# Optimization experiments

Measured on AMD Instinct MI355X. Metric: run time of the kernel, lower is better.

The kernel has to match this reference:

```python
import jax, jax.numpy as jnp
import numpy as np

B, C, H, W = 8, 512, 32, 32
HEADS, GROUPS = 8, 32
EPS = 1e-5


def setup_inputs() -> dict:
    key = jax.random.key(0)
    ks = jax.random.split(key, 6)
    s = 0.02
    return {
        "x": jax.random.normal(ks[0], (B, C, H, W), jnp.float32),
        "gn_scale": jnp.ones((C,), jnp.float32),
        "gn_bias": jnp.zeros((C,), jnp.float32),
        "wq": jax.random.normal(ks[1], (C, C), jnp.float32) * s,
        "bq": jnp.zeros((C,), jnp.float32),
        "wk": jax.random.normal(ks[2], (C, C), jnp.float32) * s,
        "bk": jnp.zeros((C,), jnp.float32),
        "wv": jax.random.normal(ks[3], (C, C), jnp.float32) * s,
        "bv": jnp.zeros((C,), jnp.float32),
        "wo": jax.random.normal(ks[4], (C, C), jnp.float32) * s,
        "bo": jnp.zeros((C,), jnp.float32),
    }


def reference(x, gn_scale, gn_bias, wq, bq, wk, bk, wv, bv, wo, bo):
    b, c, h, w = x.shape
    n = h * w
    cdh = c // HEADS
    xf = x.reshape(b, c, n)

    # GroupNorm over (channels_per_group, spatial)
    g = xf.reshape(b, GROUPS, (c // GROUPS) * n)
    mu = g.mean(-1, keepdims=True)
    var = g.var(-1, keepdims=True)
    hn = ((g - mu) * jax.lax.rsqrt(var + EPS)).reshape(b, c, n)
    hn = hn * gn_scale[:, None] + gn_bias[:, None]

    # 1x1 conv projections == channel-mixing GEMMs
    q = jnp.einsum('oc,bcn->bon', wq, hn) + bq[:, None]
    k = jnp.einsum('oc,bcn->bon', wk, hn) + bk[:, None]
    v = jnp.einsum('oc,bcn->bon', wv, hn) + bv[:, None]

    qh = q.reshape(b, HEADS, cdh, n)
    kh = k.reshape(b, HEADS, cdh, n)
    vh = v.reshape(b, HEADS, cdh, n)

    scale = 1.0 / jnp.sqrt(jnp.float32(cdh))
    scores = jnp.einsum('bhdq,bhdk->bhqk', qh, kh) * scale  # [B,H,N,N]
    attn = jax.nn.softmax(scores, axis=-1)  # dropout p=0.0 (eval) -> identity

    oh = jnp.einsum('bhqk,bhdk->bhdq', attn, vh).reshape(b, c, n)
    out = jnp.einsum('oc,bcn->bon', wo, oh) + bo[:, None]
    return (xf + out).reshape(b, c, h, w)
```

## Files before the change

kernel.cpp:

```cpp
#include <hip/hip_runtime.h>

#define BB 8
#define CC 512
#define NSP 1024
#define HEADS 8
#define DH 64
#define NGROUPS 32
#define CPG 16
#define GN_EPS 1e-5f
#define MQKV 1536

typedef __attribute__((ext_vector_type(8))) short bf16x8;
typedef __attribute__((ext_vector_type(4))) short short4v;
typedef __attribute__((ext_vector_type(4))) float f32x4;

typedef __attribute__((address_space(3))) unsigned int lds_u32;
typedef const __attribute__((address_space(1))) unsigned int glb_u32;

__device__ __forceinline__ short f2bf(float f) {
    union { float f; unsigned u; } v; v.f = f;
    unsigned r = v.u + 0x7fffu + ((v.u >> 16) & 1u);
    return (short)(r >> 16);
}
__device__ __forceinline__ short f2bf_trunc(float f) {
    union { float f; unsigned u; } v; v.f = f;
    return (short)(v.u >> 16);
}

__device__ __forceinline__ float wave_reduce_sum(float v) {
    #pragma unroll
    for (int off = 32; off > 0; off >>= 1) v += __shfl_down(v, off, 64);
    return v;
}

#define QSCALE 0.18033688011112042f

__global__ __launch_bounds__(256) void convert_w_kernel(
        const float* __restrict__ wq, const float* __restrict__ wk,
        const float* __restrict__ wv, const float* __restrict__ wo,
        const float* __restrict__ bq, const float* __restrict__ bk,
        const float* __restrict__ bv,
        short* __restrict__ wqkv, short* __restrict__ wob,
        float* __restrict__ bqkv) {
    const int gid = blockIdx.x * 256 + threadIdx.x;
    if (gid < MQKV * CC) {
        const int r = gid >> 9;
        const int cc = gid & 511;
        const float* src = (r < 512) ? wq : ((r < 1024) ? wk : wv);
        float v = src[(size_t)(r & 511) * CC + cc];
        if (r < 512) v *= QSCALE;
        wqkv[gid] = f2bf(v);
    } else {
        const int g2 = gid - MQKV * CC;
        wob[g2] = f2bf(wo[g2]);
    }
    if (gid < MQKV) {
        float bvv = (gid < 512) ? bq[gid] * QSCALE
                  : ((gid < 1024) ? bk[gid - 512] : bv[gid - 1024]);
        bqkv[gid] = bvv;
    }
}

__global__ __launch_bounds__(256) void groupnorm_t_kernel(
        const float* __restrict__ x, const float* __restrict__ gsc,
        const float* __restrict__ gbi, short* __restrict__ hnt) {
    const int b = blockIdx.x >> 5, g = blockIdx.x & 31;
    const int count = CPG * NSP;
    const size_t base = ((size_t)b * CC + (size_t)g * CPG) * NSP;
    float s = 0.f, ss = 0.f;
    for (int i = threadIdx.x; i < count; i += 256) {
        float v = x[base + i];
        s += v; ss += v * v;
    }
    __shared__ float red[2][4];
    s = wave_reduce_sum(s); ss = wave_reduce_sum(ss);
    const int wid = threadIdx.x >> 6, lane = threadIdx.x & 63;
    if (lane == 0) { red[0][wid] = s; red[1][wid] = ss; }
    __syncthreads();
    if (threadIdx.x == 0) {
        float ts  = red[0][0] + red[0][1] + red[0][2] + red[0][3];
        float tss = red[1][0] + red[1][1] + red[1][2] + red[1][3];
        float mu = ts / count;
        float var = tss / count - mu * mu;
        red[0][0] = mu;
        red[1][0] = rsqrtf(var + GN_EPS);
    }
    __syncthreads();
    const float mu = red[0][0], rstd = red[1][0];
    float sc[16], bi[16];
    #pragma unroll
    for (int ci = 0; ci < 16; ++ci) {
        sc[ci] = gsc[g * CPG + ci] * rstd;
        bi[ci] = gbi[g * CPG + ci];
    }
    for (int n0 = 0; n0 < NSP; n0 += 256) {
        const int n = n0 + threadIdx.x;
        short tmp[16];
        #pragma unroll
        for (int ci = 0; ci < 16; ++ci) {
            float v = x[base + (size_t)ci * NSP + n];
            tmp[ci] = f2bf((v - mu) * sc[ci] + bi[ci]);
        }
        const size_t ob = ((size_t)b * NSP + n) * CC + g * CPG;
        *(bf16x8*)&hnt[ob]     = *(bf16x8*)&tmp[0];
        *(bf16x8*)&hnt[ob + 8] = *(bf16x8*)&tmp[8];
    }
}

template <int MODE>
__global__ __launch_bounds__(256) void gemm_bt_kernel(
        const short* __restrict__ A, const float* __restrict__ bias,
        const short* __restrict__ Bt, void* __restrict__ Yv,
        const float* __restrict__ res, short* __restrict__ qt,
        short* __restrict__ kt, int M) {
    __shared__ short SM[2 * 128 * 64];
    short* As = SM;
    short* Bs = SM + 128 * 64;
    const int nt = blockIdx.x;
    const int b = nt >> 3, n0 = (nt & 7) * 128;
    const int o0 = blockIdx.y * 128;
    const int t = threadIdx.x, w = t >> 6, lane = t & 63;
    const int quad = lane >> 4, l16 = lane & 15;
    const int wm = w & 1, wn = w >> 1;
    const int srow = lane >> 3, scol = (lane & 7) * 8;

    f32x4 acc[4][4];
    #pragma unroll
    for (int i = 0; i < 4; ++i)
        #pragma unroll
        for (int j = 0; j < 4; ++j) acc[i][j] = (f32x4){0.f, 0.f, 0.f, 0.f};

    const short* Ab = A + (size_t)o0 * 512;
    const short* Bb = Bt + ((size_t)b * 1024 + n0) * 512;

    for (int k0 = 0; k0 < 512; k0 += 64) {
        #pragma unroll
        for (int i = 0; i < 4; ++i) {
            const int r0 = w * 32 + i * 8;
            __builtin_amdgcn_global_load_lds(
                (glb_u32*)(Ab + (size_t)(r0 + srow) * 512 + k0 + scol),
                (lds_u32*)&As[r0 * 64], 16, 0, 0);
            __builtin_amdgcn_global_load_lds(
                (glb_u32*)(Bb + (size_t)(r0 + srow) * 512 + k0 + scol),
                (lds_u32*)&Bs[r0 * 64], 16, 0, 0);
        }
        __syncthreads();

        bf16x8 af[4][2], bfr[4][2];
        #pragma unroll
        for (int mi = 0; mi < 4; ++mi)
            #pragma unroll
            for (int s = 0; s < 2; ++s)
                af[mi][s] = *(bf16x8*)&As[(wm * 64 + mi * 16 + l16) * 64 + quad * 8 + s * 32];
        #pragma unroll
        for (int ni = 0; ni < 4; ++ni)
            #pragma unroll
            for (int s = 0; s < 2; ++s)
                bfr[ni][s] = *(bf16x8*)&Bs[(wn * 64 + ni * 16 + l16) * 64 + quad * 8 + s * 32];
        #pragma unroll
        for (int mi = 0; mi < 4; ++mi)
            #pragma unroll
            for (int ni = 0; ni < 4; ++ni)
                #pragma unroll
                for (int s = 0; s < 2; ++s)
                    acc[mi][ni] = __builtin_amdgcn_mfma_f32_16x16x32_bf16(
                        af[mi][s], bfr[ni][s], acc[mi][ni], 0, 0, 0);
        __syncthreads();
    }

    if (MODE == 0 && o0 < 1024) {
        short* T = (o0 < 512) ? qt : kt;
        #pragma unroll
        for (int pass = 0; pass < 2; ++pass) {
            __syncthreads();
            if (wm == pass) {
                #pragma unroll
                for (int mi = 0; mi < 4; ++mi) {
                    const int d0 = mi * 16 + quad * 4;
                    float bv[4];
                    #pragma unroll
                    for (int r = 0; r < 4; ++r) bv[r] = bias[o0 + pass * 64 + d0 + r];
                    #pragma unroll
                    for (int ni = 0; ni < 4; ++ni) {
                        const int nl = wn * 64 + ni * 16 + l16;
                        short pk[4];
                        #pragma unroll
                        for (int r = 0; r < 4; ++r)
                            pk[r] = f2bf(acc[mi][ni][r] + bv[r]);
                        *(short4v*)&SM[nl * 68 + d0] = *(short4v*)pk;
                    }
                }
            }
            __syncthreads();
            const int hh = ((o0 & 511) >> 6) + pass;
            const size_t hb2 = ((size_t)b * HEADS + hh) * NSP;
            #pragma unroll
            for (int it = 0; it < 4; ++it) {
                const int rr = (t >> 3) + it * 32;
                const int cc = (t & 7) * 8;
                *(bf16x8*)&T[(hb2 + n0 + rr) * DH + cc] = *(bf16x8*)&SM[rr * 68 + cc];
            }
        }
        return;
    }

    #pragma unroll
    for (int mi = 0; mi < 4; ++mi) {
        #pragma unroll
        for (int r = 0; r < 4; ++r) {
            const int m = wm * 64 + mi * 16 + quad * 4 + r;
            const float bv = bias[o0 + m];
            const size_t rowb = ((size_t)b * M + o0 + m) * 1024 + n0;
            if (MODE == 0) {
                short* Y = (short*)Yv;
                #pragma unroll
                for (int ni = 0; ni < 4; ++ni) {
                    const int n = wn * 64 + ni * 16 + l16;
                    Y[rowb + n] = f2bf(acc[mi][ni][r] + bv);
                }
            } else {
                float* Y = (float*)Yv;
                #pragma unroll
                for (int ni = 0; ni < 4; ++ni) {
                    const int n = wn * 64 + ni * 16 + l16;
                    Y[rowb + n] = acc[mi][ni][r] + bv + res[rowb + n];
                }
            }
        }
    }
}

__global__ __launch_bounds__(256) void attn_mfma_kernel(
        const short* __restrict__ qkv, const short* __restrict__ qt,
        const short* __restrict__ kt, short* __restrict__ obt) {
    __shared__ short Ks[64 * 64];
    __shared__ short Vs[64 * 64];
    __shared__ short Ps[4][32][68];
    const int id = blockIdx.x;
    const int xcd = id & 7, j = id >> 3;
    const int q0 = (j & 7) * 128;
    const int hi = (j >> 3) * 8 + xcd;
    const int b = hi >> 3, h = hi & 7;
    const int t = threadIdx.x;
    const int w = t >> 6, lane = t & 63;
    const int quad = lane >> 4, l16 = lane & 15;
    const size_t vbase = ((size_t)b * MQKV + 1024 + h * DH) * NSP;
    const size_t hb = ((size_t)b * HEADS + h) * NSP;
    const int sc = (lane & 7) ^ (lane >> 3);
    const int swz0 = (quad ^ (l16 & 7)) * 8;
    const int swz1 = ((quad + 4) ^ (l16 & 7)) * 8;

    bf16x8 qf[2][2];
    #pragma unroll
    for (int g = 0; g < 2; ++g)
        #pragma unroll
        for (int s = 0; s < 2; ++s)
            qf[g][s] = *(const bf16x8*)&qt[(hb + q0 + w * 32 + g * 16 + l16) * DH
                                           + quad * 8 + 32 * s];

    float lsum[2] = {0.f, 0.f};
    f32x4 oacc[2][4];
    #pragma unroll
    for (int g = 0; g < 2; ++g)
        #pragma unroll
        for (int i = 0; i < 4; ++i) oacc[g][i] = (f32x4){0.f, 0.f, 0.f, 0.f};

    for (int k0 = 0; k0 < NSP; k0 += 64) {
        __syncthreads();
        #pragma unroll
        for (int p = 0; p < 2; ++p) {
            const int row = w * 16 + p * 8 + (lane >> 3);
            __builtin_amdgcn_global_load_lds(
                (glb_u32*)(kt + (hb + k0 + row) * DH + sc * 8),
                (lds_u32*)(Ks + w * 1024 + p * 512), 16, 0, 0);
            __builtin_amdgcn_global_load_lds(
                (glb_u32*)(qkv + vbase + (size_t)row * NSP + k0 + sc * 8),
                (lds_u32*)(Vs + w * 1024 + p * 512), 16, 0, 0);
        }
        __syncthreads();

        f32x4 st[2][4];
        #pragma unroll
        for (int ks = 0; ks < 4; ++ks) {
            bf16x8 ka0 = *(bf16x8*)&Ks[(ks * 16 + l16) * 64 + swz0];
            bf16x8 ka1 = *(bf16x8*)&Ks[(ks * 16 + l16) * 64 + swz1];
            #pragma unroll
            for (int g = 0; g < 2; ++g) {
                f32x4 a2 = (f32x4){0.f, 0.f, 0.f, 0.f};
                a2 = __builtin_amdgcn_mfma_f32_16x16x32_bf16(ka0, qf[g][0], a2, 0, 0, 0);
                a2 = __builtin_amdgcn_mfma_f32_16x16x32_bf16(ka1, qf[g][1], a2, 0, 0, 0);
                st[g][ks] = a2;
            }
        }

        #pragma unroll
        for (int g = 0; g < 2; ++g) {
            short pb[16];
            #pragma unroll
            for (int ks = 0; ks < 4; ++ks)
                #pragma unroll
                for (int r = 0; r < 4; ++r) {
                    float p = exp2f(st[g][ks][r]);
                    lsum[g] += p;
                    pb[ks * 4 + r] = f2bf_trunc(p);
                }
            #pragma unroll
            for (int ks = 0; ks < 4; ++ks)
                *(short4v*)&Ps[w][g * 16 + l16][ks * 16 + quad * 4] = *(short4v*)&pb[ks * 4];
        }
        bf16x8 pf[2][2];
        #pragma unroll
        for (int g = 0; g < 2; ++g)
            #pragma unroll
            for (int s = 0; s < 2; ++s)
                pf[g][s] = *(bf16x8*)&Ps[w][g * 16 + l16][quad * 8 + 32 * s];

        #pragma unroll
        for (int ds = 0; ds < 4; ++ds) {
            bf16x8 va0 = *(bf16x8*)&Vs[(ds * 16 + l16) * 64 + swz0];
            bf16x8 va1 = *(bf16x8*)&Vs[(ds * 16 + l16) * 64 + swz1];
            #pragma unroll
            for (int g = 0; g < 2; ++g) {
                oacc[g][ds] = __builtin_amdgcn_mfma_f32_16x16x32_bf16(va0, pf[g][0], oacc[g][ds], 0, 0, 0);
                oacc[g][ds] = __builtin_amdgcn_mfma_f32_16x16x32_bf16(va1, pf[g][1], oacc[g][ds], 0, 0, 0);
            }
        }
    }

    #pragma unroll
    for (int g = 0; g < 2; ++g) {
        float ls = lsum[g];
        ls += __shfl_xor(ls, 16, 64);
        ls += __shfl_xor(ls, 32, 64);
        const float inv = 1.0f / ls;
        const int qrow = q0 + w * 32 + g * 16 + l16;
        #pragma unroll
        for (int ds = 0; ds < 4; ++ds) {
            short o4[4];
            #pragma unroll
            for (int r = 0; r < 4; ++r) o4[r] = f2bf(oacc[g][ds][r] * inv);
            *(short4v*)&obt[((size_t)b * NSP + qrow) * CC + h * DH + ds * 16 + quad * 4] =
                *(short4v*)o4;
        }
    }
}

extern "C" void kernel_launch(void* const* d_in, const int* in_sizes, int n_in,
                              void* d_out, int out_size, void* d_ws, size_t ws_size,
                              hipStream_t stream) {
    const float* x   = (const float*)d_in[0];
    const float* gsc = (const float*)d_in[1];
    const float* gbi = (const float*)d_in[2];
    const float* wq  = (const float*)d_in[3];
    const float* bq  = (const float*)d_in[4];
    const float* wk  = (const float*)d_in[5];
    const float* bk  = (const float*)d_in[6];
    const float* wv  = (const float*)d_in[7];
    const float* bv  = (const float*)d_in[8];
    const float* wo  = (const float*)d_in[9];
    const float* bo  = (const float*)d_in[10];
    float* out = (float*)d_out;

    short* wqkv_bf = (short*)d_ws;
    short* wo_bf   = wqkv_bf + (size_t)MQKV * CC;
    float* bqkv    = (float*)(wo_bf + (size_t)CC * CC);
    short* hnt     = (short*)(bqkv + MQKV);
    short* qkv     = hnt + (size_t)BB * NSP * CC;
    short* obt     = qkv + (size_t)BB * MQKV * NSP;
    short* kt      = obt + (size_t)BB * NSP * CC;
    short* qt      = kt + (size_t)BB * HEADS * NSP * DH;

    convert_w_kernel<<<(MQKV * CC + CC * CC) / 256, 256, 0, stream>>>(
        wq, wk, wv, wo, bq, bk, bv, wqkv_bf, wo_bf, bqkv);

    groupnorm_t_kernel<<<BB * NGROUPS, 256, 0, stream>>>(x, gsc, gbi, hnt);

    dim3 qkvgrid(64, MQKV / 128);
    gemm_bt_kernel<0><<<qkvgrid, 256, 0, stream>>>(
        wqkv_bf, bqkv, hnt, (void*)qkv, nullptr, qt, kt, MQKV);

    attn_mfma_kernel<<<512, 256, 0, stream>>>(qkv, qt, kt, obt);

    dim3 wogrid(64, CC / 128);
    gemm_bt_kernel<1><<<wogrid, 256, 0, stream>>>(
        wo_bf, bo, obt, (void*)out, x, nullptr, nullptr, CC);
}
```

Measured before the change: 193.2 us.

## Fuse groupnorm with weight conversion and shrink GEMM M-tile to 64

Merges weight conversion and groupnorm into one launch. Weight conversion now uses float4 loads, and groupnorm caches each group's input slab in LDS (64KB) so x is read from global memory once instead of twice. The GEMM tile drops from 128x128 to 64x128, which doubles the grid for better CU occupancy on the small projections. The Q/K transpose epilogue now goes through a per-wave swizzled LDS staging buffer with no block-wide barriers. The tradeoffs are 64KB of LDS per groupnorm block, which limits occupancy, and less operand reuse in the GEMM.

```diff
diff --git a/kernel.cpp b/kernel.cpp
--- a/kernel.cpp
+++ b/kernel.cpp
@@ -35,49 +35,59 @@
 
 #define QSCALE 0.18033688011112042f
 
-__global__ __launch_bounds__(256) void convert_w_kernel(
+__global__ __launch_bounds__(256) void gn_conv_kernel(
+        const float* __restrict__ x, const float* __restrict__ gsc,
+        const float* __restrict__ gbi, short* __restrict__ hnt,
         const float* __restrict__ wq, const float* __restrict__ wk,
         const float* __restrict__ wv, const float* __restrict__ wo,
         const float* __restrict__ bq, const float* __restrict__ bk,
         const float* __restrict__ bv,
         short* __restrict__ wqkv, short* __restrict__ wob,
         float* __restrict__ bqkv) {
-    const int gid = blockIdx.x * 256 + threadIdx.x;
-    if (gid < MQKV * CC) {
-        const int r = gid >> 9;
-        const int cc = gid & 511;
-        const float* src = (r < 512) ? wq : ((r < 1024) ? wk : wv);
-        float v = src[(size_t)(r & 511) * CC + cc];
-        if (r < 512) v *= QSCALE;
-        wqkv[gid] = f2bf(v);
-    } else {
-        const int g2 = gid - MQKV * CC;
-        wob[g2] = f2bf(wo[g2]);
-    }
-    if (gid < MQKV) {
-        float bvv = (gid < 512) ? bq[gid] * QSCALE
-                  : ((gid < 1024) ? bk[gid - 512] : bv[gid - 1024]);
-        bqkv[gid] = bvv;
-    }
-}
-
-__global__ __launch_bounds__(256) void groupnorm_t_kernel(
-        const float* __restrict__ x, const float* __restrict__ gsc,
-        const float* __restrict__ gbi, short* __restrict__ hnt) {
+    __shared__ float xs[CPG * NSP];
+    __shared__ float red[2][4];
+    const int t = threadIdx.x;
+
+    if (blockIdx.x >= 256) {
+        const int base = (blockIdx.x - 256) * 1024 + t * 4;
+        short pk[4];
+        if (base < MQKV * CC) {
+            const int r = base >> 9, cc = base & 511;
+            const float* src = (r < 512) ? wq : ((r < 1024) ? wk : wv);
+            float4 v = *(const float4*)&src[(size_t)(r & 511) * CC + cc];
+            if (r < 512) { v.x *= QSCALE; v.y *= QSCALE; v.z *= QSCALE; v.w *= QSCALE; }
+            pk[0] = f2bf(v.x); pk[1] = f2bf(v.y); pk[2] = f2bf(v.z); pk[3] = f2bf(v.w);
+            *(short4v*)&wqkv[base] = *(short4v*)pk;
+        } else {
+            const int g2 = base - MQKV * CC;
+            float4 v = *(const float4*)&wo[g2];
+            pk[0] = f2bf(v.x); pk[1] = f2bf(v.y); pk[2] = f2bf(v.z); pk[3] = f2bf(v.w);
+            *(short4v*)&wob[g2] = *(short4v*)pk;
+        }
+        const int fid = (blockIdx.x - 256) * 256 + t;
+        if (fid < MQKV) {
+            float bvv = (fid < 512) ? bq[fid] * QSCALE
+                      : ((fid < 1024) ? bk[fid - 512] : bv[fid - 1024]);
+            bqkv[fid] = bvv;
+        }
+        return;
+    }
+
     const int b = blockIdx.x >> 5, g = blockIdx.x & 31;
     const int count = CPG * NSP;
     const size_t base = ((size_t)b * CC + (size_t)g * CPG) * NSP;
     float s = 0.f, ss = 0.f;
-    for (int i = threadIdx.x; i < count; i += 256) {
-        float v = x[base + i];
-        s += v; ss += v * v;
-    }
-    __shared__ float red[2][4];
+    for (int i = t * 4; i < count; i += 1024) {
+        float4 v = *(const float4*)&x[base + i];
+        *(float4*)&xs[i] = v;
+        s += v.x + v.y + v.z + v.w;
+        ss += v.x * v.x + v.y * v.y + v.z * v.z + v.w * v.w;
+    }
     s = wave_reduce_sum(s); ss = wave_reduce_sum(ss);
-    const int wid = threadIdx.x >> 6, lane = threadIdx.x & 63;
+    const int wid = t >> 6, lane = t & 63;
     if (lane == 0) { red[0][wid] = s; red[1][wid] = ss; }
     __syncthreads();
-    if (threadIdx.x == 0) {
+    if (t == 0) {
         float ts  = red[0][0] + red[0][1] + red[0][2] + red[0][3];
         float tss = red[1][0] + red[1][1] + red[1][2] + red[1][3];
         float mu = ts / count;
@@ -94,11 +104,11 @@
         bi[ci] = gbi[g * CPG + ci];
     }
     for (int n0 = 0; n0 < NSP; n0 += 256) {
-        const int n = n0 + threadIdx.x;
+        const int n = n0 + t;
         short tmp[16];
         #pragma unroll
         for (int ci = 0; ci < 16; ++ci) {
-            float v = x[base + (size_t)ci * NSP + n];
+            float v = xs[ci * NSP + n];
             tmp[ci] = f2bf((v - mu) * sc[ci] + bi[ci]);
         }
         const size_t ob = ((size_t)b * NSP + n) * CC + g * CPG;
@@ -113,54 +123,56 @@
         const short* __restrict__ Bt, void* __restrict__ Yv,
         const float* __restrict__ res, short* __restrict__ qt,
         short* __restrict__ kt, int M) {
-    __shared__ short SM[2 * 128 * 64];
-    short* As = SM;
-    short* Bs = SM + 128 * 64;
+    __shared__ short As[64 * 64];
+    __shared__ short Bs[128 * 64];
     const int nt = blockIdx.x;
     const int b = nt >> 3, n0 = (nt & 7) * 128;
-    const int o0 = blockIdx.y * 128;
+    const int o0 = blockIdx.y * 64;
     const int t = threadIdx.x, w = t >> 6, lane = t & 63;
     const int quad = lane >> 4, l16 = lane & 15;
-    const int wm = w & 1, wn = w >> 1;
-    const int srow = lane >> 3, scol = (lane & 7) * 8;
-
-    f32x4 acc[4][4];
+
+    f32x4 acc[4][2];
     #pragma unroll
     for (int i = 0; i < 4; ++i)
         #pragma unroll
-        for (int j = 0; j < 4; ++j) acc[i][j] = (f32x4){0.f, 0.f, 0.f, 0.f};
+        for (int j = 0; j < 2; ++j) acc[i][j] = (f32x4){0.f, 0.f, 0.f, 0.f};
 
     const short* Ab = A + (size_t)o0 * 512;
     const short* Bb = Bt + ((size_t)b * 1024 + n0) * 512;
+    const int lrow = lane >> 3, lch = lane & 7;
 
     for (int k0 = 0; k0 < 512; k0 += 64) {
         #pragma unroll
-        for (int i = 0; i < 4; ++i) {
-            const int r0 = w * 32 + i * 8;
+        for (int p = 0; p < 2; ++p) {
+            const int row = w * 16 + p * 8 + lrow;
             __builtin_amdgcn_global_load_lds(
-                (glb_u32*)(Ab + (size_t)(r0 + srow) * 512 + k0 + scol),
-                (lds_u32*)&As[r0 * 64], 16, 0, 0);
+                (glb_u32*)(Ab + (size_t)row * 512 + k0 + lch * 8),
+                (lds_u32*)&As[(w * 2 + p) * 512], 16, 0, 0);
+        }
+        #pragma unroll
+        for (int p = 0; p < 4; ++p) {
+            const int row = w * 32 + p * 8 + lrow;
             __builtin_amdgcn_global_load_lds(
-                (glb_u32*)(Bb + (size_t)(r0 + srow) * 512 + k0 + scol),
-                (lds_u32*)&Bs[r0 * 64], 16, 0, 0);
+                (glb_u32*)(Bb + (size_t)row * 512 + k0 + lch * 8),
+                (lds_u32*)&Bs[(w * 4 + p) * 512], 16, 0, 0);
         }
         __syncthreads();
 
-        bf16x8 af[4][2], bfr[4][2];
+        bf16x8 af[4][2], bfr[2][2];
         #pragma unroll
         for (int mi = 0; mi < 4; ++mi)
             #pragma unroll
             for (int s = 0; s < 2; ++s)
-                af[mi][s] = *(bf16x8*)&As[(wm * 64 + mi * 16 + l16) * 64 + quad * 8 + s * 32];
-        #pragma unroll
-        for (int ni = 0; ni < 4; ++ni)
+                af[mi][s] = *(bf16x8*)&As[(mi * 16 + l16) * 64 + quad * 8 + s * 32];
+        #pragma unroll
+        for (int ni = 0; ni < 2; ++ni)
             #pragma unroll
             for (int s = 0; s < 2; ++s)
-                bfr[ni][s] = *(bf16x8*)&Bs[(wn * 64 + ni * 16 + l16) * 64 + quad * 8 + s * 32];
+                bfr[ni][s] = *(bf16x8*)&Bs[(w * 32 + ni * 16 + l16) * 64 + quad * 8 + s * 32];
         #pragma unroll
         for (int mi = 0; mi < 4; ++mi)
             #pragma unroll
-            for (int ni = 0; ni < 4; ++ni)
+            for (int ni = 0; ni < 2; ++ni)
                 #pragma unroll
                 for (int s = 0; s < 2; ++s)
                     acc[mi][ni] = __builtin_amdgcn_mfma_f32_16x16x32_bf16(
@@ -170,36 +182,30 @@
 
     if (MODE == 0 && o0 < 1024) {
         short* T = (o0 < 512) ? qt : kt;
-        #pragma unroll
-        for (int pass = 0; pass < 2; ++pass) {
-            __syncthreads();
-            if (wm == pass) {
-                #pragma unroll
-                for (int mi = 0; mi < 4; ++mi) {
-                    const int d0 = mi * 16 + quad * 4;
-                    float bv[4];
-                    #pragma unroll
-                    for (int r = 0; r < 4; ++r) bv[r] = bias[o0 + pass * 64 + d0 + r];
-                    #pragma unroll
-                    for (int ni = 0; ni < 4; ++ni) {
-                        const int nl = wn * 64 + ni * 16 + l16;
-                        short pk[4];
-                        #pragma unroll
-                        for (int r = 0; r < 4; ++r)
-                            pk[r] = f2bf(acc[mi][ni][r] + bv[r]);
-                        *(short4v*)&SM[nl * 68 + d0] = *(short4v*)pk;
-                    }
-                }
+        const int hh = (o0 & 511) >> 6;
+        const size_t hb2 = ((size_t)b * HEADS + hh) * NSP;
+        short* Ts = Bs + w * 2048;
+        #pragma unroll
+        for (int mi = 0; mi < 4; ++mi) {
+            const int d0 = mi * 16 + quad * 4;
+            const int c = d0 >> 3, dlo = d0 & 7;
+            float bv[4];
+            #pragma unroll
+            for (int r = 0; r < 4; ++r) bv[r] = bias[o0 + d0 + r];
+            #pragma unroll
+            for (int ni = 0; ni < 2; ++ni) {
+                const int nl = ni * 16 + l16;
+                short pk[4];
+                #pragma unroll
+                for (int r = 0; r < 4; ++r) pk[r] = f2bf(acc[mi][ni][r] + bv[r]);
+                *(short4v*)&Ts[nl * 64 + ((c ^ (nl & 7)) * 8) + dlo] = *(short4v*)pk;
             }
-            __syncthreads();
-            const int hh = ((o0 & 511) >> 6) + pass;
-            const size_t hb2 = ((size_t)b * HEADS + hh) * NSP;
-            #pragma unroll
-            for (int it = 0; it < 4; ++it) {
-                const int rr = (t >> 3) + it * 32;
-                const int cc = (t & 7) * 8;
-                *(bf16x8*)&T[(hb2 + n0 + rr) * DH + cc] = *(bf16x8*)&SM[rr * 68 + cc];
-            }
+        }
+        #pragma unroll
+        for (int it = 0; it < 4; ++it) {
+            const int rr = lrow + it * 8;
+            bf16x8 vv = *(bf16x8*)&Ts[rr * 64 + ((lch ^ (rr & 7)) * 8)];
+            *(bf16x8*)&T[(hb2 + n0 + w * 32 + rr) * DH + lch * 8] = vv;
         }
         return;
     }
@@ -208,21 +214,21 @@
     for (int mi = 0; mi < 4; ++mi) {
         #pragma unroll
         for (int r = 0; r < 4; ++r) {
-            const int m = wm * 64 + mi * 16 + quad * 4 + r;
+            const int m = mi * 16 + quad * 4 + r;
             const float bv = bias[o0 + m];
             const size_t rowb = ((size_t)b * M + o0 + m) * 1024 + n0;
             if (MODE == 0) {
                 short* Y = (short*)Yv;
                 #pragma unroll
-                for (int ni = 0; ni < 4; ++ni) {
-                    const int n = wn * 64 + ni * 16 + l16;
+                for (int ni = 0; ni < 2; ++ni) {
+                    const int n = w * 32 + ni * 16 + l16;
                     Y[rowb + n] = f2bf(acc[mi][ni][r] + bv);
                 }
             } else {
                 float* Y = (float*)Yv;
                 #pragma unroll
-                for (int ni = 0; ni < 4; ++ni) {
-                    const int n = wn * 64 + ni * 16 + l16;
+                for (int ni = 0; ni < 2; ++ni) {
+                    const int n = w * 32 + ni * 16 + l16;
                     Y[rowb + n] = acc[mi][ni][r] + bv + res[rowb + n];
                 }
             }
@@ -370,18 +376,16 @@
     short* kt      = obt + (size_t)BB * NSP * CC;
     short* qt      = kt + (size_t)BB * HEADS * NSP * DH;
 
-    convert_w_kernel<<<(MQKV * CC + CC * CC) / 256, 256, 0, stream>>>(
-        wq, wk, wv, wo, bq, bk, bv, wqkv_bf, wo_bf, bqkv);
-
-    groupnorm_t_kernel<<<BB * NGROUPS, 256, 0, stream>>>(x, gsc, gbi, hnt);
-
-    dim3 qkvgrid(64, MQKV / 128);
+    gn_conv_kernel<<<1280, 256, 0, stream>>>(
+        x, gsc, gbi, hnt, wq, wk, wv, wo, bq, bk, bv, wqkv_bf, wo_bf, bqkv);
+
+    dim3 qkvgrid(64, MQKV / 64);
     gemm_bt_kernel<0><<<qkvgrid, 256, 0, stream>>>(
         wqkv_bf, bqkv, hnt, (void*)qkv, nullptr, qt, kt, MQKV);
 
     attn_mfma_kernel<<<512, 256, 0, stream>>>(qkv, qt, kt, obt);
 
-    dim3 wogrid(64, CC / 128);
+    dim3 wogrid(64, CC / 64);
     gemm_bt_kernel<1><<<wogrid, 256, 0, stream>>>(
         wo_bf, bo, obt, (void*)out, x, nullptr, nullptr, CC);
 }
```

Result: faster. 165.8 us (-14.2%).
